# Optimization experiments

Hardware: AMD Instinct MI355X
Metric: run time of the kernel (lower is better)

The kernel has to match this reference:

```python
import jax, jax.numpy as jnp
import numpy as np

SIZE = 128   # feature dim
N = 4096     # number of mesh nodes


def setup_inputs() -> dict:
    key = jax.random.key(0)
    k_f, k_adj, k_q, k_k = jax.random.split(key, 4)
    # f: [size, N] node features (features-first, as in the torch module); scaled
    # so QK dot products stay O(1) and exp() is numerically safe.
    f = jax.random.normal(k_f, (SIZE, N), dtype=jnp.float32) * 0.1
    # neighbors: [N, N] binary adjacency with self-loops (every row sums > 0).
    adj = (jax.random.uniform(k_adj, (N, N)) < 0.005).astype(jnp.float32)
    neighbors = jnp.maximum(adj, jnp.eye(N, dtype=jnp.float32))
    # learned per-feature scale vectors (nn.init.normal_)
    wq = jax.random.normal(k_q, (SIZE,), dtype=jnp.float32)
    wk = jax.random.normal(k_k, (SIZE,), dtype=jnp.float32)
    return {"f": f, "neighbors": neighbors, "wq": wq, "wk": wk}


def reference(f, neighbors, wq, wk):
    # elementwise-scaled queries/keys: [size, N]
    wq_f = wq[:, None] * f
    wk_f = wk[:, None] * f
    # S[i, j] = exp(<wq_f[:, i], wk_f[:, j]>)  -> [N, N]
    S = jnp.exp(jnp.einsum('dn,dm->nm', wq_f, wk_f))
    # normalize by neighbor-sums: S / (neighbors @ S).T
    S = S / jnp.matmul(neighbors, S).T
    return S
```

## Files before the change

### kernel.cpp

```cpp
#include <hip/hip_runtime.h>

#define N    4096
#define SIZE 128
#define CAP  128
#define RB   16
#define TB   1024

typedef __attribute__((ext_vector_type(8))) short bf16x8;
typedef __attribute__((ext_vector_type(4))) float f32x4;

__device__ __forceinline__ unsigned int bf16rne(float x) {
    union { float f; unsigned int u; } c; c.f = x;
    return (c.u + 0x7fffu + ((c.u >> 16) & 1u)) >> 16;
}
__device__ __forceinline__ short bf16s(float x) { return (short)bf16rne(x); }
__device__ __forceinline__ float bflo(unsigned int u) {
    union { unsigned int u; float f; } c; c.u = u << 16; return c.f;
}
__device__ __forceinline__ float bfhi(unsigned int u) {
    union { unsigned int u; float f; } c; c.u = u & 0xffff0000u; return c.f;
}

__global__ __launch_bounds__(256)
void build_csr(const float* __restrict__ nb, int* __restrict__ cnt4,
               int* __restrict__ idx) {
    __shared__ int sc;
    const int j    = blockIdx.x;
    const int lane = threadIdx.x & 63;
    if (threadIdx.x == 0) sc = 0;
    __syncthreads();
    const float4* row4 = (const float4*)(nb + (size_t)j * N);
    int* irow = idx + (size_t)j * CAP;

    float4 v[4];
#pragma unroll
    for (int it = 0; it < 4; ++it) v[it] = row4[threadIdx.x + it * 256];

#pragma unroll
    for (int it = 0; it < 4; ++it) {
        const float e[4] = {v[it].x, v[it].y, v[it].z, v[it].w};
#pragma unroll
        for (int q = 0; q < 4; ++q) {
            const bool nz = (e[q] != 0.0f);
            const unsigned long long m = __ballot(nz);
            if (m != 0ull) {
                int base = 0;
                if (lane == 0) base = atomicAdd(&sc, __popcll(m));
                base = __shfl(base, 0);
                if (nz) {
                    const int p = base + __popcll(m & ((1ull << lane) - 1ull));
                    const int c = 4 * (threadIdx.x + it * 256) + q;
                    if (p < CAP) irow[p] = c;
                }
            }
        }
    }
    __syncthreads();
    if (threadIdx.x == 0) {
        int n  = (sc < CAP) ? sc : CAP;
        int n4 = (n + 3) & ~3;
        for (int p = n; p < n4; ++p) irow[p] = N;
        cnt4[j] = n4 >> 2;
    }
}

__global__ __launch_bounds__(256)
void prep(const float* __restrict__ f, const float* __restrict__ wq,
          const float* __restrict__ wk, short* __restrict__ qwfA,
          short* __restrict__ fB) {
    const int tid  = blockIdx.x * 256 + threadIdx.x;
    const int half = tid >> 16;
    const int id   = tid & 65535;
    const int grp  = id >> 6;
    const int lane = id & 63;
    const int tile = grp >> 2;
    const int ks   = grp & 3;
    const int quad = lane >> 4;
    const int col  = lane & 15;
    bf16x8 v;
    if (half == 0) {
#pragma unroll
        for (int jj = 0; jj < 8; ++jj) {
            const int k = ks * 32 + quad * 8 + jj;
            v[jj] = bf16s(wq[k] * wk[k] * f[(size_t)k * N + tile * 16 + col]);
        }
        ((bf16x8*)qwfA)[id] = v;
    } else {
#pragma unroll
        for (int jj = 0; jj < 8; ++jj) {
            const int k = ks * 32 + quad * 8 + jj;
            v[jj] = bf16s(f[(size_t)k * N + tile * 16 + col]);
        }
        ((bf16x8*)fB)[id] = v;
    }
}

__global__ __launch_bounds__(TB, 4)
void fused(const short* __restrict__ qwfA, const short* __restrict__ fB,
           const int* __restrict__ cnt4, const int* __restrict__ idx,
           float* __restrict__ out) {
    __shared__ uint4 sA[N + 1];
    __shared__ uint4 sB[N + 1];
    const int t    = threadIdx.x;
    const int lane = t & 63;
    const int wv   = t >> 6;
    const int quad = lane >> 4;
    const int i0   = blockIdx.x * RB;

    bf16x8 af[4];
    const bf16x8* Ap = (const bf16x8*)qwfA + (size_t)blockIdx.x * 4 * 64;
#pragma unroll
    for (int ks = 0; ks < 4; ++ks) af[ks] = Ap[ks * 64 + lane];
    const bf16x8* Bp = (const bf16x8*)fB;

#pragma unroll 4
    for (int ti = 0; ti < 16; ++ti) {
        const int nt = wv * 16 + ti;
        f32x4 acc = {0.f, 0.f, 0.f, 0.f};
#pragma unroll
        for (int ks = 0; ks < 4; ++ks) {
            const bf16x8 bfrag = Bp[(size_t)(nt * 4 + ks) * 64 + lane];
            acc = __builtin_amdgcn_mfma_f32_16x16x32_bf16(af[ks], bfrag, acc, 0, 0, 0);
        }
        const int j = nt * 16 + (lane & 15);
        uint2 p;
        p.x = bf16rne(__expf(acc[0])) | (bf16rne(__expf(acc[1])) << 16);
        p.y = bf16rne(__expf(acc[2])) | (bf16rne(__expf(acc[3])) << 16);
        uint2* base = (quad < 2) ? (uint2*)&sA[j] : (uint2*)&sB[j];
        base[quad & 1] = p;
    }
    if (t == 0) {
        sA[N] = make_uint4(0u, 0u, 0u, 0u);
        sB[N] = make_uint4(0u, 0u, 0u, 0u);
    }
    __syncthreads();

    for (int u = 0; u < N / TB; ++u) {
        const int j  = t + u * TB;
        const int c4 = cnt4[j];
        const int4* irow = (const int4*)(idx + (size_t)j * CAP);
        float den[RB];
#pragma unroll
        for (int r = 0; r < RB; ++r) den[r] = 0.0f;

        int4 k = irow[0];
        for (int c = 0; c < c4; ++c) {
            const int4 kn = (c + 1 < c4) ? irow[c + 1] : k;
            const uint4 a0 = sA[k.x], b0 = sB[k.x];
            const uint4 a1 = sA[k.y], b1 = sB[k.y];
            const uint4 a2 = sA[k.z], b2 = sB[k.z];
            const uint4 a3 = sA[k.w], b3 = sB[k.w];
            den[0]  += bflo(a0.x) + bflo(a1.x) + bflo(a2.x) + bflo(a3.x);
            den[1]  += bfhi(a0.x) + bfhi(a1.x) + bfhi(a2.x) + bfhi(a3.x);
            den[2]  += bflo(a0.y) + bflo(a1.y) + bflo(a2.y) + bflo(a3.y);
            den[3]  += bfhi(a0.y) + bfhi(a1.y) + bfhi(a2.y) + bfhi(a3.y);
            den[4]  += bflo(a0.z) + bflo(a1.z) + bflo(a2.z) + bflo(a3.z);
            den[5]  += bfhi(a0.z) + bfhi(a1.z) + bfhi(a2.z) + bfhi(a3.z);
            den[6]  += bflo(a0.w) + bflo(a1.w) + bflo(a2.w) + bflo(a3.w);
            den[7]  += bfhi(a0.w) + bfhi(a1.w) + bfhi(a2.w) + bfhi(a3.w);
            den[8]  += bflo(b0.x) + bflo(b1.x) + bflo(b2.x) + bflo(b3.x);
            den[9]  += bfhi(b0.x) + bfhi(b1.x) + bfhi(b2.x) + bfhi(b3.x);
            den[10] += bflo(b0.y) + bflo(b1.y) + bflo(b2.y) + bflo(b3.y);
            den[11] += bfhi(b0.y) + bfhi(b1.y) + bfhi(b2.y) + bfhi(b3.y);
            den[12] += bflo(b0.z) + bflo(b1.z) + bflo(b2.z) + bflo(b3.z);
            den[13] += bfhi(b0.z) + bfhi(b1.z) + bfhi(b2.z) + bfhi(b3.z);
            den[14] += bflo(b0.w) + bflo(b1.w) + bflo(b2.w) + bflo(b3.w);
            den[15] += bfhi(b0.w) + bfhi(b1.w) + bfhi(b2.w) + bfhi(b3.w);
            k = kn;
        }
        const uint4 na = sA[j], nb = sB[j];
        const float nums[RB] = {
            bflo(na.x), bfhi(na.x), bflo(na.y), bfhi(na.y),
            bflo(na.z), bfhi(na.z), bflo(na.w), bfhi(na.w),
            bflo(nb.x), bfhi(nb.x), bflo(nb.y), bfhi(nb.y),
            bflo(nb.z), bfhi(nb.z), bflo(nb.w), bfhi(nb.w)};
#pragma unroll
        for (int r = 0; r < RB; ++r)
            out[(size_t)(i0 + r) * N + j] = nums[r] * __builtin_amdgcn_rcpf(den[r]);
    }
}

extern "C" void kernel_launch(void* const* d_in, const int* in_sizes, int n_in,
                              void* d_out, int out_size, void* d_ws, size_t ws_size,
                              hipStream_t stream) {
    const float* f  = (const float*)d_in[0];
    const float* nb = (const float*)d_in[1];
    const float* wq = (const float*)d_in[2];
    const float* wk = (const float*)d_in[3];
    float* out = (float*)d_out;

    int*   cnt4 = (int*)d_ws;
    int*   idx  = cnt4 + N;
    short* qwfA = (short*)(idx + (size_t)N * CAP);
    short* fB   = qwfA + (size_t)256 * 4 * 64 * 8;

    prep<<<512, 256, 0, stream>>>(f, wq, wk, qwfA, fB);
    build_csr<<<N, 256, 0, stream>>>(nb, cnt4, idx);
    fused<<<N / RB, TB, 0, stream>>>(qwfA, fB, cnt4, idx, out);
}
```

Before: 169.5 us.

## Switch to fp16 storage with packed half2 denominator accumulation and tiled prep

Replaces bf16 with fp16 for the MFMA operands and the stored exp values, converting with the packed round-toward-zero instruction. Neighbor-sum accumulation now uses packed half2 adds split across two accumulator sets, roughly halving the ALU work in the gather loop compared with per-element bf16-to-float unpacking. The prep kernel stages f through shared memory and writes both operand layouts from one block per tile, and the shared-memory buffers are merged and offset. fp16 accumulation of up to 128 exp terms risks precision loss or overflow when exp values are large.

```diff
diff --git a/kernel.cpp b/kernel.cpp
--- a/kernel.cpp
+++ b/kernel.cpp
@@ -1,4 +1,5 @@
 #include <hip/hip_runtime.h>
+#include <hip/hip_fp16.h>
 
 #define N    4096
 #define SIZE 128
@@ -6,19 +7,17 @@
 #define RB   16
 #define TB   1024
 
-typedef __attribute__((ext_vector_type(8))) short bf16x8;
+typedef __attribute__((ext_vector_type(8))) _Float16 f16x8;
+typedef __attribute__((ext_vector_type(2))) __fp16 fp16x2;
 typedef __attribute__((ext_vector_type(4))) float f32x4;
 
-__device__ __forceinline__ unsigned int bf16rne(float x) {
-    union { float f; unsigned int u; } c; c.f = x;
-    return (c.u + 0x7fffu + ((c.u >> 16) & 1u)) >> 16;
-}
-__device__ __forceinline__ short bf16s(float x) { return (short)bf16rne(x); }
-__device__ __forceinline__ float bflo(unsigned int u) {
-    union { unsigned int u; float f; } c; c.u = u << 16; return c.f;
-}
-__device__ __forceinline__ float bfhi(unsigned int u) {
-    union { unsigned int u; float f; } c; c.u = u & 0xffff0000u; return c.f;
+__device__ __forceinline__ unsigned int pk2(float lo, float hi) {
+    union { fp16x2 v; unsigned int u; } c;
+    c.v = __builtin_amdgcn_cvt_pkrtz(lo, hi);
+    return c.u;
+}
+__device__ __forceinline__ __half2 u2h(unsigned int u) {
+    union { unsigned int u; __half2 h; } c; c.u = u; return c.h;
 }
 
 __global__ __launch_bounds__(256)
@@ -66,52 +65,56 @@
 
 __global__ __launch_bounds__(256)
 void prep(const float* __restrict__ f, const float* __restrict__ wq,
-          const float* __restrict__ wk, short* __restrict__ qwfA,
-          short* __restrict__ fB) {
-    const int tid  = blockIdx.x * 256 + threadIdx.x;
-    const int half = tid >> 16;
-    const int id   = tid & 65535;
-    const int grp  = id >> 6;
-    const int lane = id & 63;
-    const int tile = grp >> 2;
-    const int ks   = grp & 3;
+          const float* __restrict__ wk, _Float16* __restrict__ Af,
+          _Float16* __restrict__ Bf) {
+    __shared__ float sf[SIZE][16];
+    __shared__ float sqw[SIZE];
+    const int t    = threadIdx.x;
+    const int tile = blockIdx.x;
+    if (t < SIZE) sqw[t] = wq[t] * wk[t];
+    const int col0 = t & 15;
+#pragma unroll
+    for (int it = 0; it < 8; ++it) {
+        const int k = (t >> 4) + it * 16;
+        sf[k][col0] = f[(size_t)k * N + tile * 16 + col0];
+    }
+    __syncthreads();
+
+    const int ks   = t >> 6;
+    const int lane = t & 63;
     const int quad = lane >> 4;
     const int col  = lane & 15;
-    bf16x8 v;
-    if (half == 0) {
-#pragma unroll
-        for (int jj = 0; jj < 8; ++jj) {
-            const int k = ks * 32 + quad * 8 + jj;
-            v[jj] = bf16s(wq[k] * wk[k] * f[(size_t)k * N + tile * 16 + col]);
-        }
-        ((bf16x8*)qwfA)[id] = v;
-    } else {
-#pragma unroll
-        for (int jj = 0; jj < 8; ++jj) {
-            const int k = ks * 32 + quad * 8 + jj;
-            v[jj] = bf16s(f[(size_t)k * N + tile * 16 + col]);
-        }
-        ((bf16x8*)fB)[id] = v;
-    }
+    f16x8 va, vb;
+#pragma unroll
+    for (int jj = 0; jj < 8; ++jj) {
+        const int k = ks * 32 + quad * 8 + jj;
+        const float v = sf[k][col];
+        va[jj] = (_Float16)(sqw[k] * v);
+        vb[jj] = (_Float16)v;
+    }
+    const size_t o = (size_t)(tile * 4 + ks) * 64 + lane;
+    ((f16x8*)Af)[o] = va;
+    ((f16x8*)Bf)[o] = vb;
 }
 
 __global__ __launch_bounds__(TB, 4)
-void fused(const short* __restrict__ qwfA, const short* __restrict__ fB,
+void fused(const _Float16* __restrict__ Af, const _Float16* __restrict__ Bf,
            const int* __restrict__ cnt4, const int* __restrict__ idx,
            float* __restrict__ out) {
-    __shared__ uint4 sA[N + 1];
-    __shared__ uint4 sB[N + 1];
+    __shared__ uint4 Sb[2 * N + 3];
+    uint4* const sA = Sb;
+    uint4* const sB = Sb + N + 2;
     const int t    = threadIdx.x;
     const int lane = t & 63;
     const int wv   = t >> 6;
     const int quad = lane >> 4;
     const int i0   = blockIdx.x * RB;
 
-    bf16x8 af[4];
-    const bf16x8* Ap = (const bf16x8*)qwfA + (size_t)blockIdx.x * 4 * 64;
+    f16x8 af[4];
+    const f16x8* Ap = (const f16x8*)Af + (size_t)blockIdx.x * 4 * 64;
 #pragma unroll
     for (int ks = 0; ks < 4; ++ks) af[ks] = Ap[ks * 64 + lane];
-    const bf16x8* Bp = (const bf16x8*)fB;
+    const f16x8* Bp = (const f16x8*)Bf;
 
 #pragma unroll 4
     for (int ti = 0; ti < 16; ++ti) {
@@ -119,13 +122,13 @@
         f32x4 acc = {0.f, 0.f, 0.f, 0.f};
 #pragma unroll
         for (int ks = 0; ks < 4; ++ks) {
-            const bf16x8 bfrag = Bp[(size_t)(nt * 4 + ks) * 64 + lane];
-            acc = __builtin_amdgcn_mfma_f32_16x16x32_bf16(af[ks], bfrag, acc, 0, 0, 0);
+            const f16x8 bfrag = Bp[(size_t)(nt * 4 + ks) * 64 + lane];
+            acc = __builtin_amdgcn_mfma_f32_16x16x32_f16(af[ks], bfrag, acc, 0, 0, 0);
         }
         const int j = nt * 16 + (lane & 15);
         uint2 p;
-        p.x = bf16rne(__expf(acc[0])) | (bf16rne(__expf(acc[1])) << 16);
-        p.y = bf16rne(__expf(acc[2])) | (bf16rne(__expf(acc[3])) << 16);
+        p.x = pk2(__expf(acc[0]), __expf(acc[1]));
+        p.y = pk2(__expf(acc[2]), __expf(acc[3]));
         uint2* base = (quad < 2) ? (uint2*)&sA[j] : (uint2*)&sB[j];
         base[quad & 1] = p;
     }
@@ -139,44 +142,47 @@
         const int j  = t + u * TB;
         const int c4 = cnt4[j];
         const int4* irow = (const int4*)(idx + (size_t)j * CAP);
-        float den[RB];
-#pragma unroll
-        for (int r = 0; r < RB; ++r) den[r] = 0.0f;
+        __half2 d0[8], d1[8];
+        const __half2 z = u2h(0u);
+#pragma unroll
+        for (int r = 0; r < 8; ++r) { d0[r] = z; d1[r] = z; }
 
         int4 k = irow[0];
         for (int c = 0; c < c4; ++c) {
             const int4 kn = (c + 1 < c4) ? irow[c + 1] : k;
-            const uint4 a0 = sA[k.x], b0 = sB[k.x];
-            const uint4 a1 = sA[k.y], b1 = sB[k.y];
-            const uint4 a2 = sA[k.z], b2 = sB[k.z];
-            const uint4 a3 = sA[k.w], b3 = sB[k.w];
-            den[0]  += bflo(a0.x) + bflo(a1.x) + bflo(a2.x) + bflo(a3.x);
-            den[1]  += bfhi(a0.x) + bfhi(a1.x) + bfhi(a2.x) + bfhi(a3.x);
-            den[2]  += bflo(a0.y) + bflo(a1.y) + bflo(a2.y) + bflo(a3.y);
-            den[3]  += bfhi(a0.y) + bfhi(a1.y) + bfhi(a2.y) + bfhi(a3.y);
-            den[4]  += bflo(a0.z) + bflo(a1.z) + bflo(a2.z) + bflo(a3.z);
-            den[5]  += bfhi(a0.z) + bfhi(a1.z) + bfhi(a2.z) + bfhi(a3.z);
-            den[6]  += bflo(a0.w) + bflo(a1.w) + bflo(a2.w) + bflo(a3.w);
-            den[7]  += bfhi(a0.w) + bfhi(a1.w) + bfhi(a2.w) + bfhi(a3.w);
-            den[8]  += bflo(b0.x) + bflo(b1.x) + bflo(b2.x) + bflo(b3.x);
-            den[9]  += bfhi(b0.x) + bfhi(b1.x) + bfhi(b2.x) + bfhi(b3.x);
-            den[10] += bflo(b0.y) + bflo(b1.y) + bflo(b2.y) + bflo(b3.y);
-            den[11] += bfhi(b0.y) + bfhi(b1.y) + bfhi(b2.y) + bfhi(b3.y);
-            den[12] += bflo(b0.z) + bflo(b1.z) + bflo(b2.z) + bflo(b3.z);
-            den[13] += bfhi(b0.z) + bfhi(b1.z) + bfhi(b2.z) + bfhi(b3.z);
-            den[14] += bflo(b0.w) + bflo(b1.w) + bflo(b2.w) + bflo(b3.w);
-            den[15] += bfhi(b0.w) + bfhi(b1.w) + bfhi(b2.w) + bfhi(b3.w);
+            const uint4 ax = sA[k.x], bx = sB[k.x];
+            const uint4 ay = sA[k.y], by = sB[k.y];
+            const uint4 az = sA[k.z], bz = sB[k.z];
+            const uint4 aw = sA[k.w], bw = sB[k.w];
+            d0[0] = __hadd2(d0[0], u2h(ax.x)); d1[0] = __hadd2(d1[0], u2h(ay.x));
+            d0[1] = __hadd2(d0[1], u2h(ax.y)); d1[1] = __hadd2(d1[1], u2h(ay.y));
+            d0[2] = __hadd2(d0[2], u2h(ax.z)); d1[2] = __hadd2(d1[2], u2h(ay.z));
+            d0[3] = __hadd2(d0[3], u2h(ax.w)); d1[3] = __hadd2(d1[3], u2h(ay.w));
+            d0[4] = __hadd2(d0[4], u2h(bx.x)); d1[4] = __hadd2(d1[4], u2h(by.x));
+            d0[5] = __hadd2(d0[5], u2h(bx.y)); d1[5] = __hadd2(d1[5], u2h(by.y));
+            d0[6] = __hadd2(d0[6], u2h(bx.z)); d1[6] = __hadd2(d1[6], u2h(by.z));
+            d0[7] = __hadd2(d0[7], u2h(bx.w)); d1[7] = __hadd2(d1[7], u2h(by.w));
+            d0[0] = __hadd2(d0[0], u2h(az.x)); d1[0] = __hadd2(d1[0], u2h(aw.x));
+            d0[1] = __hadd2(d0[1], u2h(az.y)); d1[1] = __hadd2(d1[1], u2h(aw.y));
+            d0[2] = __hadd2(d0[2], u2h(az.z)); d1[2] = __hadd2(d1[2], u2h(aw.z));
+            d0[3] = __hadd2(d0[3], u2h(az.w)); d1[3] = __hadd2(d1[3], u2h(aw.w));
+            d0[4] = __hadd2(d0[4], u2h(bz.x)); d1[4] = __hadd2(d1[4], u2h(bw.x));
+            d0[5] = __hadd2(d0[5], u2h(bz.y)); d1[5] = __hadd2(d1[5], u2h(bw.y));
+            d0[6] = __hadd2(d0[6], u2h(bz.z)); d1[6] = __hadd2(d1[6], u2h(bw.z));
+            d0[7] = __hadd2(d0[7], u2h(bz.w)); d1[7] = __hadd2(d1[7], u2h(bw.w));
             k = kn;
         }
         const uint4 na = sA[j], nb = sB[j];
-        const float nums[RB] = {
-            bflo(na.x), bfhi(na.x), bflo(na.y), bfhi(na.y),
-            bflo(na.z), bfhi(na.z), bflo(na.w), bfhi(na.w),
-            bflo(nb.x), bfhi(nb.x), bflo(nb.y), bfhi(nb.y),
-            bflo(nb.z), bfhi(nb.z), bflo(nb.w), bfhi(nb.w)};
-#pragma unroll
-        for (int r = 0; r < RB; ++r)
-            out[(size_t)(i0 + r) * N + j] = nums[r] * __builtin_amdgcn_rcpf(den[r]);
+        const unsigned int nu[8] = {na.x, na.y, na.z, na.w, nb.x, nb.y, nb.z, nb.w};
+#pragma unroll
+        for (int i = 0; i < 8; ++i) {
+            const __half2 dd = __hadd2(d0[i], d1[i]);
+            const __half2 nn = u2h(nu[i]);
+            out[(size_t)(i0 + 2 * i + 0) * N + j] =
+                __low2float(nn)  * __builtin_amdgcn_rcpf(__low2float(dd));
+            out[(size_t)(i0 + 2 * i + 1) * N + j] =
+                __high2float(nn) * __builtin_amdgcn_rcpf(__high2float(dd));
+        }
     }
 }
 
@@ -189,12 +195,12 @@
     const float* wk = (const float*)d_in[3];
     float* out = (float*)d_out;
 
-    int*   cnt4 = (int*)d_ws;
-    int*   idx  = cnt4 + N;
-    short* qwfA = (short*)(idx + (size_t)N * CAP);
-    short* fB   = qwfA + (size_t)256 * 4 * 64 * 8;
-
-    prep<<<512, 256, 0, stream>>>(f, wq, wk, qwfA, fB);
+    int*      cnt4 = (int*)d_ws;
+    int*      idx  = cnt4 + N;
+    _Float16* Af   = (_Float16*)(idx + (size_t)N * CAP);
+    _Float16* Bf   = Af + (size_t)256 * 4 * 64 * 8;
+
     build_csr<<<N, 256, 0, stream>>>(nb, cnt4, idx);
-    fused<<<N / RB, TB, 0, stream>>>(qwfA, fB, cnt4, idx, out);
-}
+    prep<<<256, 256, 0, stream>>>(f, wq, wk, Af, Bf);
+    fused<<<N / RB, TB, 0, stream>>>(Af, Bf, cnt4, idx, out);
+}
```

Result: no change. 168.0 us (-0.9%).
